# Kernel optimization log

Hardware: AMD Instinct MI355X
Metric: run time of the kernel (lower is better)

The kernel has to match this reference:

```python
import jax, jax.numpy as jnp
import numpy as np
from functools import partial

L, H, D, HD, V, S_MAX = 12, 12, 768, 64, 50257, 1024
EPS = 1e-5


def _layernorm(x, g, b):
    m = jnp.mean(x, axis=-1, keepdims=True)
    v = jnp.mean(jnp.square(x - m), axis=-1, keepdims=True)
    return (x - m) * jax.lax.rsqrt(v + EPS) * g + b


def setup_inputs() -> dict:
    key = jax.random.key(0)
    ks = jax.random.split(key, 8)
    s = 0.02
    return {
        "input_ids": jax.random.randint(ks[0], (2, 1024), 0, V),
        "wte": jax.random.normal(ks[1], (V, D), jnp.float32) * s,
        "wpe": jax.random.normal(ks[2], (S_MAX, D), jnp.float32) * s,
        "ln1_g": jnp.ones((L, D), jnp.float32),
        "ln1_b": jnp.zeros((L, D), jnp.float32),
        "Wqkv": jax.random.normal(ks[3], (L, D, 3 * D), jnp.float32) * s,
        "bqkv": jnp.zeros((L, 3 * D), jnp.float32),
        "Wo": jax.random.normal(ks[4], (L, D, D), jnp.float32) * s,
        "bo": jnp.zeros((L, D), jnp.float32),
        "ln2_g": jnp.ones((L, D), jnp.float32),
        "ln2_b": jnp.zeros((L, D), jnp.float32),
        "Wfc": jax.random.normal(ks[5], (L, D, 4 * D), jnp.float32) * s,
        "bfc": jnp.zeros((L, 4 * D), jnp.float32),
        "Wp": jax.random.normal(ks[6], (L, 4 * D, D), jnp.float32) * s,
        "bp": jnp.zeros((L, D), jnp.float32),
        "lnf_g": jnp.ones((D,), jnp.float32),
        "lnf_b": jnp.zeros((D,), jnp.float32),
    }


def reference(input_ids, wte, wpe, ln1_g, ln1_b, Wqkv, bqkv, Wo, bo,
              ln2_g, ln2_b, Wfc, bfc, Wp, bp, lnf_g, lnf_b):
    B, S = input_ids.shape
    x = wte[input_ids] + wpe[:S][None]  # [B,S,D] (embd dropout = identity in eval)
    causal = jnp.tril(jnp.ones((S, S), bool))  # [S,S]
    scale = 1.0 / jnp.sqrt(jnp.asarray(HD, x.dtype))

    def block(x, p):
        l1g, l1b, wqkv, bq, wo, bo_, l2g, l2b, wfc, bfc_, wp, bp_ = p
        h = _layernorm(x, l1g, l1b)
        qkv = h @ wqkv + bq  # [B,S,3D]
        q, k, v = jnp.split(qkv, 3, axis=-1)
        q = q.reshape(B, S, H, HD).transpose(0, 2, 1, 3)  # [B,H,S,HD]
        k = k.reshape(B, S, H, HD).transpose(0, 2, 1, 3)
        v = v.reshape(B, S, H, HD).transpose(0, 2, 1, 3)
        scores = jnp.einsum('bhqd,bhkd->bhqk', q, k) * scale  # [B,H,S,S]
        scores = jnp.where(causal, scores, -jnp.inf)
        attn = jax.nn.softmax(scores, axis=-1)  # attn dropout = identity in eval
        o = jnp.einsum('bhqk,bhkd->bhqd', attn, v)
        o = o.transpose(0, 2, 1, 3).reshape(B, S, D)
        x = x + (o @ wo + bo_)
        h2 = _layernorm(x, l2g, l2b)
        m = jax.nn.gelu(h2 @ wfc + bfc_, approximate=False)  # exact erf GELU
        x = x + (m @ wp + bp_)
        return x, None

    params = (ln1_g, ln1_b, Wqkv, bqkv, Wo, bo, ln2_g, ln2_b, Wfc, bfc, Wp, bp)
    x, _ = jax.lax.scan(block, x, params)
    x = _layernorm(x, lnf_g, lnf_b)
    logits = jnp.einsum('bsd,vd->bsv', x, wte)  # tied lm_head, no bias
    return logits
```

## Files before the change

### kernel.cpp

```cpp
#include <hip/hip_runtime.h>
#include <hip/hip_bf16.h>
#include <hip/hip_fp16.h>


typedef __attribute__((ext_vector_type(8))) short short8;
typedef __attribute__((ext_vector_type(4))) float f32x4;

#define S_LEN  1024
#define NTOK   2048
#define DMODEL 768
#define NHEAD  12
#define HEADD  64
#define NLAYER 12
#define VOCAB  50257
#define DQKV   2304
#define DFF    3072

__device__ __forceinline__ unsigned short f2bf(float f) {
  unsigned u = __float_as_uint(f);
  u += 0x7fffu + ((u >> 16) & 1u);
  return (unsigned short)(u >> 16);
}
__device__ __forceinline__ unsigned short f2h(float f) {
  __half h = __float2half(f);
  return *reinterpret_cast<unsigned short*>(&h);
}

__device__ __forceinline__ f32x4 mfma_bf16(short8 a, short8 b, f32x4 c) {
  asm("v_mfma_f32_16x16x32_bf16 %0, %1, %2, %0" : "+v"(c) : "v"(a), "v"(b));
  return c;
}
__device__ __forceinline__ f32x4 mfma_f16(short8 a, short8 b, f32x4 c) {
  asm("v_mfma_f32_16x16x32_f16 %0, %1, %2, %0" : "+v"(c) : "v"(a), "v"(b));
  return c;
}

__device__ __forceinline__ void gll16(const void* g, void* l) {
  __builtin_amdgcn_global_load_lds(
      (const __attribute__((address_space(1))) void*)g,
      (__attribute__((address_space(3))) void*)l, 16, 0, 0);
}

__global__ __launch_bounds__(256) void embed_kernel(
    const int* __restrict__ ids, const float* __restrict__ wte,
    const float* __restrict__ wpe, float* __restrict__ x) {
  int i = blockIdx.x * 256 + threadIdx.x;
  int n = i / DMODEL, d = i - n * DMODEL;
  int s = n & (S_LEN - 1);
  x[i] = wte[(long)ids[n] * DMODEL + d] + wpe[(long)s * DMODEL + d];
}

__global__ __launch_bounds__(256) void convert_kernel(
    const float* __restrict__ in, unsigned short* __restrict__ out, long n4) {
  long i = (long)blockIdx.x * 256 + threadIdx.x;
  if (i >= n4) return;
  float4 v = ((const float4*)in)[i];
  ushort4 r;
  r.x = f2bf(v.x); r.y = f2bf(v.y); r.z = f2bf(v.z); r.w = f2bf(v.w);
  ((ushort4*)out)[i] = r;
}

__global__ __launch_bounds__(256) void transpose_kernel(
    const float* __restrict__ in, unsigned short* __restrict__ out, int R, int C,
    long ldin, long ldout) {
  in  += (long)blockIdx.z * ldin;
  out += (long)blockIdx.z * ldout;
  __shared__ float tile[32][33];
  int tx = threadIdx.x & 31, ty = threadIdx.x >> 5;
  int c0 = blockIdx.x * 32, r0 = blockIdx.y * 32;
#pragma unroll
  for (int i = 0; i < 4; ++i) {
    int r = r0 + ty + i * 8;
    tile[ty + i * 8][tx] = in[(long)r * C + c0 + tx];
  }
  __syncthreads();
#pragma unroll
  for (int i = 0; i < 4; ++i) {
    int orow = c0 + ty + i * 8;
    out[(long)orow * R + r0 + tx] = f2bf(tile[tx][ty + i * 8]);
  }
}

__global__ __launch_bounds__(256) void ln_kernel(
    const float* __restrict__ x, const float* __restrict__ g,
    const float* __restrict__ b, unsigned short* __restrict__ out) {
  __shared__ float sb[4];
  int n = blockIdx.x, t = threadIdx.x;
  const float* xr = x + (long)n * DMODEL;
  float v0 = xr[t], v1 = xr[t + 256], v2 = xr[t + 512];
  float sum = v0 + v1 + v2;
#pragma unroll
  for (int o = 32; o; o >>= 1) sum += __shfl_xor(sum, o);
  if ((t & 63) == 0) sb[t >> 6] = sum;
  __syncthreads();
  sum = sb[0] + sb[1] + sb[2] + sb[3];
  float mean = sum * (1.f / 768.f);
  float d0 = v0 - mean, d1 = v1 - mean, d2 = v2 - mean;
  float vs = d0 * d0 + d1 * d1 + d2 * d2;
#pragma unroll
  for (int o = 32; o; o >>= 1) vs += __shfl_xor(vs, o);
  __syncthreads();
  if ((t & 63) == 0) sb[t >> 6] = vs;
  __syncthreads();
  vs = sb[0] + sb[1] + sb[2] + sb[3];
  float rs = rsqrtf(vs * (1.f / 768.f) + 1e-5f);
  out[(long)n * DMODEL + t]       = f2bf(d0 * rs * g[t] + b[t]);
  out[(long)n * DMODEL + t + 256] = f2bf(d1 * rs * g[t + 256] + b[t + 256]);
  out[(long)n * DMODEL + t + 512] = f2bf(d2 * rs * g[t + 512] + b[t + 512]);
}

__global__ __launch_bounds__(256) void attn_kernel(
    const unsigned short* __restrict__ qkv, unsigned short* __restrict__ o_out) {
  __shared__ __align__(16) unsigned short Ks[64 * 64];
  __shared__ __align__(16) unsigned short Vt[64 * 64];
  __shared__ __align__(16) unsigned short Ps[4][16 * 72];
  int t = threadIdx.x, w = t >> 6, l = t & 63;
  int qtile = blockIdx.x, bh = blockIdx.y;
  int b = bh / NHEAD, h = bh - b * NHEAD;
  long nb = (long)b * S_LEN;
  int g = l >> 4, lr = l & 15;

  int q0 = qtile * 64 + w * 16;
  const unsigned short* qrow = qkv + (nb + q0 + lr) * (long)DQKV + h * HEADD;
  short8 qf0 = *(const short8*)(qrow + g * 8);
  short8 qf1 = *(const short8*)(qrow + 32 + g * 8);

  f32x4 O[4];
  f32x4 zero = {0.f, 0.f, 0.f, 0.f};
#pragma unroll
  for (int jt = 0; jt < 4; ++jt) O[jt] = zero;
  float m[4] = {-INFINITY, -INFINITY, -INFINITY, -INFINITY};
  float ls[4] = {0.f, 0.f, 0.f, 0.f};

  int skey = t >> 2;
  int sd0 = (t & 3) * 16;
  int nt = qtile + 1;
  for (int c = 0; c < nt; ++c) {
    int k0 = c * 64;
    __syncthreads();
    {
      int c0 = t, row = c0 >> 3, j = c0 & 7;
      long goff = (nb + k0 + row) * (long)DQKV + DMODEL + h * HEADD + ((j ^ (row & 7)) * 8);
      gll16(qkv + goff, (char*)Ks + c0 * 16);
      int c1 = t + 256; row = c1 >> 3; j = c1 & 7;
      goff = (nb + k0 + row) * (long)DQKV + DMODEL + h * HEADD + ((j ^ (row & 7)) * 8);
      gll16(qkv + goff, (char*)Ks + c1 * 16);
    }
    {
      const unsigned short* vr =
          qkv + (nb + k0 + skey) * (long)DQKV + 2 * DMODEL + h * HEADD + sd0;
      short8 v0 = *(const short8*)vr;
      short8 v1 = *(const short8*)(vr + 8);
#pragma unroll
      for (int j = 0; j < 8; ++j) {
        int dv = sd0 + j;
        *(unsigned short*)((char*)Vt + dv * 128 + ((skey * 2) ^ ((dv & 7) << 4))) =
            (unsigned short)v0[j];
        dv = sd0 + 8 + j;
        *(unsigned short*)((char*)Vt + dv * 128 + ((skey * 2) ^ ((dv & 7) << 4))) =
            (unsigned short)v1[j];
      }
    }
    __syncthreads();

    f32x4 S[4];
#pragma unroll
    for (int kt = 0; kt < 4; ++kt) {
      int krow = kt * 16 + lr;
      int o0 = (g * 16) ^ ((krow & 7) << 4);
      int o1 = (64 + g * 16) ^ ((krow & 7) << 4);
      short8 kf0 = *(const short8*)((char*)Ks + krow * 128 + o0);
      short8 kf1 = *(const short8*)((char*)Ks + krow * 128 + o1);
      S[kt] = mfma_f16(qf0, kf0, zero);
      S[kt] = mfma_f16(qf1, kf1, S[kt]);
    }

    bool diag = (c == qtile);
    float sv[4][4];
#pragma unroll
    for (int kt = 0; kt < 4; ++kt)
#pragma unroll
      for (int r = 0; r < 4; ++r) {
        float xv = S[kt][r] * 0.125f;
        if (diag) {
          int key = kt * 16 + lr;
          int qq = w * 16 + g * 4 + r;
          if (key > qq) xv = -INFINITY;
        }
        sv[kt][r] = xv;
      }
    float nm[4], al[4];
#pragma unroll
    for (int r = 0; r < 4; ++r) {
      float mx = fmaxf(fmaxf(sv[0][r], sv[1][r]), fmaxf(sv[2][r], sv[3][r]));
#pragma unroll
      for (int o = 8; o; o >>= 1) mx = fmaxf(mx, __shfl_xor(mx, o));
      nm[r] = fmaxf(m[r], mx);
      al[r] = __expf(m[r] - nm[r]);
      m[r] = nm[r];
    }
    float rs[4] = {0.f, 0.f, 0.f, 0.f};
#pragma unroll
    for (int kt = 0; kt < 4; ++kt)
#pragma unroll
      for (int r = 0; r < 4; ++r) {
        float p = __expf(sv[kt][r] - nm[r]);
        rs[r] += p;
        Ps[w][(g * 4 + r) * 72 + kt * 16 + lr] = f2bf(p);
      }
#pragma unroll
    for (int r = 0; r < 4; ++r) {
#pragma unroll
      for (int o = 8; o; o >>= 1) rs[r] += __shfl_xor(rs[r], o);
      ls[r] = ls[r] * al[r] + rs[r];
    }
#pragma unroll
    for (int jt = 0; jt < 4; ++jt) {
      f32x4 ov = O[jt];
#pragma unroll
      for (int r = 0; r < 4; ++r) ov[r] *= al[r];
      O[jt] = ov;
    }
#pragma unroll
    for (int kk = 0; kk < 2; ++kk) {
      short8 pf = *(const short8*)(&Ps[w][lr * 72 + kk * 32 + g * 8]);
#pragma unroll
      for (int jt = 0; jt < 4; ++jt) {
        int dv = jt * 16 + lr;
        short8 vf = *(const short8*)((char*)Vt + dv * 128 +
                                     (((kk * 64 + g * 16)) ^ ((dv & 7) << 4)));
        O[jt] = mfma_bf16(pf, vf, O[jt]);
      }
    }
  }

  __syncthreads();
#pragma unroll
  for (int jt = 0; jt < 4; ++jt)
#pragma unroll
    for (int r = 0; r < 4; ++r) {
      int qq = w * 16 + g * 4 + r;
      int dv = jt * 16 + lr;
      *(unsigned short*)((char*)Ks + qq * 128 + ((dv * 2) ^ ((qq & 7) << 4))) =
          f2bf(O[jt][r] / ls[r]);
    }
  __syncthreads();
  {
    int qq = t >> 2, d0 = (t & 3) * 16;
    short8 o0 = *(const short8*)((char*)Ks + qq * 128 + ((d0 * 2) ^ ((qq & 7) << 4)));
    short8 o1 = *(const short8*)((char*)Ks + qq * 128 + (((d0 + 8) * 2) ^ ((qq & 7) << 4)));
    unsigned short* orow = o_out + (nb + qtile * 64 + qq) * (long)DMODEL + h * HEADD + d0;
    *(short8*)orow = o0;
    *(short8*)(orow + 8) = o1;
  }
}

template <int TM, int TN, int HAS_BIAS, int ACT_GELU, int RESID, int OUT_BF16,
          int OUT_QKV, int COLG, int GRIDSWAP, int XCDSWZ>
__global__ __launch_bounds__(TM == 128 ? 256 : 128) void gemm_bt_kernel(
    const short* __restrict__ A, const short* __restrict__ Bt,
    const float* __restrict__ bias, float* __restrict__ Cf,
    unsigned short* __restrict__ Cb, int K, int Nv) {
  __shared__ __align__(16) short As[TM * 32];
  __shared__ __align__(16) short Bs[TN * 32];
  constexpr int NJ = (TN == 64) ? 2 : 4;
  constexpr int WN = (TN == 64) ? 32 : 64;
  int t = threadIdx.x;
  int lane = t & 63, wave = t >> 6;
  int wm = (TM == 128) ? (wave >> 1) : 0;
  int wn = (TM == 128) ? (wave & 1) : wave;

  int bx = blockIdx.x, by = blockIdx.y;
  if (XCDSWZ) {
    int gx = gridDim.x;
    int nwg = gx * gridDim.y;
    int wg = by * gx + bx;
    int q8 = nwg >> 3, r8 = nwg & 7;
    int xcd = wg & 7, idx = wg >> 3;
    int nid = (xcd < r8 ? xcd * (q8 + 1) : r8 * (q8 + 1) + (xcd - r8) * q8) + idx;
    bx = nid % gx;
    by = nid / gx;
  }
  int row0 = (GRIDSWAP ? bx : by) * TM;
  int col0 = (GRIDSWAP ? by : bx) * TN;
  int lr = lane & 15, lk = (lane >> 4) * 8;

  f32x4 acc[4][NJ];
  f32x4 zero = {0.f, 0.f, 0.f, 0.f};
#pragma unroll
  for (int i = 0; i < 4; ++i)
#pragma unroll
    for (int j = 0; j < NJ; ++j) acc[i][j] = zero;

  int rr = t >> 2, k8 = (t & 3) * 8;

  if (TM == 128) {
    int ar0 = row0 + rr, ar1 = ar0 + 64;
    int br0 = col0 + rr, br1 = br0 + 64;
    if (COLG) { br0 = min(br0, Nv - 1); br1 = min(br1, Nv - 1); }
    const short* Ap0 = A + (long)ar0 * K + k8;
    const short* Ap1 = A + (long)ar1 * K + k8;
    const short* Bp0 = Bt + (long)br0 * K + k8;
    const short* Bp1 = Bt + (long)br1 * K + k8;
    for (int kt = 0; kt < K; kt += 32) {
      __syncthreads();
      gll16(Ap0 + kt, (char*)As + t * 16);
      gll16(Ap1 + kt, (char*)As + 4096 + t * 16);
      gll16(Bp0 + kt, (char*)Bs + t * 16);
      gll16(Bp1 + kt, (char*)Bs + 4096 + t * 16);
      __syncthreads();
      short8 af[4], bfr[4];
#pragma unroll
      for (int i = 0; i < 4; ++i) {
        af[i]  = *(const short8*)(As + (wm * 64 + i * 16 + lr) * 32 + lk);
        bfr[i] = *(const short8*)(Bs + (wn * 64 + i * 16 + lr) * 32 + lk);
      }
#pragma unroll
      for (int i = 0; i < 4; ++i)
#pragma unroll
        for (int j = 0; j < 4; ++j)
          acc[i][j] = mfma_bf16(af[i], bfr[j], acc[i][j]);
    }
  } else if (TN == 128) {
    const short* Ap = A + (long)(row0 + rr) * K + k8;
    const short* Bp = Bt + (long)(col0 + rr) * K + k8;
    for (int kt = 0; kt < K; kt += 32) {
      __syncthreads();
      gll16(Ap + kt, (char*)As + t * 16);
      gll16(Ap + (long)32 * K + kt, (char*)As + 2048 + t * 16);
      gll16(Bp + kt, (char*)Bs + t * 16);
      gll16(Bp + (long)32 * K + kt, (char*)Bs + 2048 + t * 16);
      gll16(Bp + (long)64 * K + kt, (char*)Bs + 4096 + t * 16);
      gll16(Bp + (long)96 * K + kt, (char*)Bs + 6144 + t * 16);
      __syncthreads();
      short8 af[4], bfr[4];
#pragma unroll
      for (int i = 0; i < 4; ++i) {
        af[i]  = *(const short8*)(As + (i * 16 + lr) * 32 + lk);
        bfr[i] = *(const short8*)(Bs + (wn * 64 + i * 16 + lr) * 32 + lk);
      }
#pragma unroll
      for (int i = 0; i < 4; ++i)
#pragma unroll
        for (int j = 0; j < 4; ++j)
          acc[i][j] = mfma_bf16(af[i], bfr[j], acc[i][j]);
    }
  } else {
    const short* Ap = A + (long)(row0 + rr) * K + k8;
    const short* Bp = Bt + (long)(col0 + rr) * K + k8;
    for (int kt = 0; kt < K; kt += 32) {
      __syncthreads();
      gll16(Ap + kt, (char*)As + t * 16);
      gll16(Ap + (long)32 * K + kt, (char*)As + 2048 + t * 16);
      gll16(Bp + kt, (char*)Bs + t * 16);
      gll16(Bp + (long)32 * K + kt, (char*)Bs + 2048 + t * 16);
      __syncthreads();
      short8 af[4], bfr[2];
#pragma unroll
      for (int i = 0; i < 4; ++i)
        af[i] = *(const short8*)(As + (i * 16 + lr) * 32 + lk);
#pragma unroll
      for (int j = 0; j < 2; ++j)
        bfr[j] = *(const short8*)(Bs + (wn * 32 + j * 16 + lr) * 32 + lk);
#pragma unroll
      for (int i = 0; i < 4; ++i)
#pragma unroll
        for (int j = 0; j < 2; ++j)
          acc[i][j] = mfma_bf16(af[i], bfr[j], acc[i][j]);
    }
  }

  int orow = row0 + wm * 64 + (lane >> 4) * 4;
  int ocol = col0 + wn * WN + lr;
#pragma unroll
  for (int i = 0; i < 4; ++i) {
#pragma unroll
    for (int j = 0; j < NJ; ++j) {
      int col = ocol + j * 16;
      if (COLG && col >= Nv) continue;
      float bv = 0.f;
      if (HAS_BIAS) bv = bias[col];
#pragma unroll
      for (int r = 0; r < 4; ++r) {
        float xv = acc[i][j][r] + bv;
        if (ACT_GELU) xv = 0.5f * xv * (1.f + erff(xv * 0.70710678118654752f));
        long idx = (long)(orow + i * 16 + r) * Nv + col;
        if (RESID) {
          Cf[idx] += xv;
        } else if (OUT_QKV) {
          Cb[idx] = (col < 2 * DMODEL) ? f2h(xv) : f2bf(xv);
        } else if (OUT_BF16) {
          Cb[idx] = f2bf(xv);
        } else {
          Cf[idx] = xv;
        }
      }
    }
  }
}

extern "C" void kernel_launch(void* const* d_in, const int* in_sizes, int n_in,
                              void* d_out, int out_size, void* d_ws, size_t ws_size,
                              hipStream_t stream) {
  const int*   ids  = (const int*)d_in[0];
  const float* wte  = (const float*)d_in[1];
  const float* wpe  = (const float*)d_in[2];
  const float* ln1g = (const float*)d_in[3];
  const float* ln1b = (const float*)d_in[4];
  const float* Wqkv = (const float*)d_in[5];
  const float* bqkv = (const float*)d_in[6];
  const float* Wo   = (const float*)d_in[7];
  const float* bo   = (const float*)d_in[8];
  const float* ln2g = (const float*)d_in[9];
  const float* ln2b = (const float*)d_in[10];
  const float* Wfc  = (const float*)d_in[11];
  const float* bfc  = (const float*)d_in[12];
  const float* Wp   = (const float*)d_in[13];
  const float* bp   = (const float*)d_in[14];
  const float* lnfg = (const float*)d_in[15];
  const float* lnfb = (const float*)d_in[16];
  float* out = (float*)d_out;

  size_t off = 0;
  auto carve = [&](size_t bytes) {
    void* p = (char*)d_ws + off;
    off += (bytes + 255) & ~(size_t)255;
    return p;
  };
  float* x = (float*)carve((size_t)NTOK * DMODEL * 4);
  unsigned short* qkvb = (unsigned short*)carve((size_t)NTOK * DQKV * 2);
  unsigned short* h    = (unsigned short*)carve((size_t)NTOK * DMODEL * 2);
  unsigned short* ob   = (unsigned short*)carve((size_t)NTOK * DMODEL * 2);
  unsigned short* mb   = (unsigned short*)carve((size_t)NTOK * DFF * 2);
  unsigned short* wteb = (unsigned short*)carve((size_t)VOCAB * DMODEL * 2);

  const size_t szQ = (size_t)DMODEL * DQKV * 2, szO = (size_t)DMODEL * DMODEL * 2;
  const size_t szF = (size_t)DMODEL * DFF * 2,  szP = (size_t)DFF * DMODEL * 2;
  size_t fixed_end = off;
  size_t full_need = fixed_end + NLAYER * (szQ + szO + szF + szP) + 4 * 256;
  bool full = ws_size >= full_need;

  unsigned short *tQ, *tO, *tF, *tP;
  if (full) {
    tQ = (unsigned short*)carve(NLAYER * szQ);
    tO = (unsigned short*)carve(NLAYER * szO);
    tF = (unsigned short*)carve(NLAYER * szF);
    tP = (unsigned short*)carve(NLAYER * szP);
  } else {
    tQ = (unsigned short*)carve(szQ);
    tO = (unsigned short*)carve(szO);
    tF = (unsigned short*)carve(szF);
    tP = (unsigned short*)carve(szP);
  }
  if (off > ws_size) return;

  dim3 blk(256), blk128(128);
  long n4 = (long)VOCAB * DMODEL / 4;
  convert_kernel<<<dim3((unsigned)((n4 + 255) / 256)), blk, 0, stream>>>(wte, wteb, n4);
  embed_kernel<<<dim3(NTOK * DMODEL / 256), blk, 0, stream>>>(ids, wte, wpe, x);

  if (full) {
    transpose_kernel<<<dim3(DQKV / 32, DMODEL / 32, NLAYER), blk, 0, stream>>>(
        Wqkv, tQ, DMODEL, DQKV, (long)DMODEL * DQKV, (long)DMODEL * DQKV);
    transpose_kernel<<<dim3(DMODEL / 32, DMODEL / 32, NLAYER), blk, 0, stream>>>(
        Wo, tO, DMODEL, DMODEL, (long)DMODEL * DMODEL, (long)DMODEL * DMODEL);
    transpose_kernel<<<dim3(DFF / 32, DMODEL / 32, NLAYER), blk, 0, stream>>>(
        Wfc, tF, DMODEL, DFF, (long)DMODEL * DFF, (long)DMODEL * DFF);
    transpose_kernel<<<dim3(DMODEL / 32, DFF / 32, NLAYER), blk, 0, stream>>>(
        Wp, tP, DFF, DMODEL, (long)DFF * DMODEL, (long)DFF * DMODEL);
  }

  for (int l = 0; l < NLAYER; ++l) {
    const unsigned short* tQl = tQ + (full ? (size_t)l * DMODEL * DQKV : 0);
    const unsigned short* tOl = tO + (full ? (size_t)l * DMODEL * DMODEL : 0);
    const unsigned short* tFl = tF + (full ? (size_t)l * DMODEL * DFF : 0);
    const unsigned short* tPl = tP + (full ? (size_t)l * DFF * DMODEL : 0);
    if (!full) {
      transpose_kernel<<<dim3(DQKV / 32, DMODEL / 32), blk, 0, stream>>>(
          Wqkv + (long)l * DMODEL * DQKV, tQ, DMODEL, DQKV, 0, 0);
      transpose_kernel<<<dim3(DMODEL / 32, DMODEL / 32), blk, 0, stream>>>(
          Wo + (long)l * DMODEL * DMODEL, tO, DMODEL, DMODEL, 0, 0);
      transpose_kernel<<<dim3(DFF / 32, DMODEL / 32), blk, 0, stream>>>(
          Wfc + (long)l * DMODEL * DFF, tF, DMODEL, DFF, 0, 0);
      transpose_kernel<<<dim3(DMODEL / 32, DFF / 32), blk, 0, stream>>>(
          Wp + (long)l * DFF * DMODEL, tP, DFF, DMODEL, 0, 0);
    }

    ln_kernel<<<dim3(NTOK), blk, 0, stream>>>(x, ln1g + l * DMODEL, ln1b + l * DMODEL, h);
    gemm_bt_kernel<64, 128, 1, 0, 0, 0, 1, 0, 0, 0>
        <<<dim3(DQKV / 128, NTOK / 64), blk128, 0, stream>>>(
        (const short*)h, (const short*)tQl, bqkv + (long)l * DQKV,
        nullptr, qkvb, DMODEL, DQKV);

    attn_kernel<<<dim3(S_LEN / 64, 2 * NHEAD), blk, 0, stream>>>(qkvb, ob);

    gemm_bt_kernel<64, 64, 1, 0, 1, 0, 0, 0, 0, 0>
        <<<dim3(DMODEL / 64, NTOK / 64), blk128, 0, stream>>>(
        (const short*)ob, (const short*)tOl, bo + (long)l * DMODEL,
        x, nullptr, DMODEL, DMODEL);

    ln_kernel<<<dim3(NTOK), blk, 0, stream>>>(x, ln2g + l * DMODEL, ln2b + l * DMODEL, h);
    gemm_bt_kernel<64, 128, 1, 1, 0, 1, 0, 0, 0, 0>
        <<<dim3(DFF / 128, NTOK / 64), blk128, 0, stream>>>(
        (const short*)h, (const short*)tFl, bfc + (long)l * DFF,
        nullptr, mb, DMODEL, DFF);

    gemm_bt_kernel<64, 64, 1, 0, 1, 0, 0, 0, 0, 0>
        <<<dim3(DMODEL / 64, NTOK / 64), blk128, 0, stream>>>(
        (const short*)mb, (const short*)tPl, bp + (long)l * DMODEL,
        x, nullptr, DFF, DMODEL);
  }

  ln_kernel<<<dim3(NTOK), blk, 0, stream>>>(x, lnfg, lnfb, h);
  gemm_bt_kernel<128, 128, 0, 0, 0, 0, 0, 1, 1, 1>
      <<<dim3(NTOK / 128, (VOCAB + 127) / 128), blk, 0, stream>>>(
      (const short*)h, (const short*)wteb, nullptr, out, nullptr, DMODEL, VOCAB);
}
```

Baseline: 2.560 ms.

## Use fp16 for attention PV and load two K-slices per GEMM barrier

```diff
diff --git a/kernel.cpp b/kernel.cpp
--- a/kernel.cpp
+++ b/kernel.cpp
@@ -206,7 +206,7 @@
       for (int r = 0; r < 4; ++r) {
         float p = __expf(sv[kt][r] - nm[r]);
         rs[r] += p;
-        Ps[w][(g * 4 + r) * 72 + kt * 16 + lr] = f2bf(p);
+        Ps[w][(g * 4 + r) * 72 + kt * 16 + lr] = f2h(p);
       }
 #pragma unroll
     for (int r = 0; r < 4; ++r) {
@@ -229,7 +229,7 @@
         int dv = jt * 16 + lr;
         short8 vf = *(const short8*)((char*)Vt + dv * 128 +
                                      (((kk * 64 + g * 16)) ^ ((dv & 7) << 4)));
-        O[jt] = mfma_bf16(pf, vf, O[jt]);
+        O[jt] = mfma_f16(pf, vf, O[jt]);
       }
     }
   }
@@ -256,13 +256,13 @@
 }
 
 template <int TM, int TN, int HAS_BIAS, int ACT_GELU, int RESID, int OUT_BF16,
-          int OUT_QKV, int COLG, int GRIDSWAP, int XCDSWZ>
+          int OUT_F16, int COLG, int GRIDSWAP, int XCDSWZ>
 __global__ __launch_bounds__(TM == 128 ? 256 : 128) void gemm_bt_kernel(
     const short* __restrict__ A, const short* __restrict__ Bt,
     const float* __restrict__ bias, float* __restrict__ Cf,
     unsigned short* __restrict__ Cb, int K, int Nv) {
-  __shared__ __align__(16) short As[TM * 32];
-  __shared__ __align__(16) short Bs[TN * 32];
+  __shared__ __align__(16) short As[2][TM * 32];
+  __shared__ __align__(16) short Bs[2][TN * 32];
   constexpr int NJ = (TN == 64) ? 2 : 4;
   constexpr int WN = (TN == 64) ? 32 : 64;
   int t = threadIdx.x;
@@ -302,71 +302,92 @@
     const short* Ap1 = A + (long)ar1 * K + k8;
     const short* Bp0 = Bt + (long)br0 * K + k8;
     const short* Bp1 = Bt + (long)br1 * K + k8;
-    for (int kt = 0; kt < K; kt += 32) {
+    for (int kt = 0; kt < K; kt += 64) {
       __syncthreads();
-      gll16(Ap0 + kt, (char*)As + t * 16);
-      gll16(Ap1 + kt, (char*)As + 4096 + t * 16);
-      gll16(Bp0 + kt, (char*)Bs + t * 16);
-      gll16(Bp1 + kt, (char*)Bs + 4096 + t * 16);
+      gll16(Ap0 + kt, (char*)As[0] + t * 16);
+      gll16(Ap1 + kt, (char*)As[0] + 4096 + t * 16);
+      gll16(Bp0 + kt, (char*)Bs[0] + t * 16);
+      gll16(Bp1 + kt, (char*)Bs[0] + 4096 + t * 16);
+      gll16(Ap0 + kt + 32, (char*)As[1] + t * 16);
+      gll16(Ap1 + kt + 32, (char*)As[1] + 4096 + t * 16);
+      gll16(Bp0 + kt + 32, (char*)Bs[1] + t * 16);
+      gll16(Bp1 + kt + 32, (char*)Bs[1] + 4096 + t * 16);
       __syncthreads();
-      short8 af[4], bfr[4];
-#pragma unroll
-      for (int i = 0; i < 4; ++i) {
-        af[i]  = *(const short8*)(As + (wm * 64 + i * 16 + lr) * 32 + lk);
-        bfr[i] = *(const short8*)(Bs + (wn * 64 + i * 16 + lr) * 32 + lk);
-      }
-#pragma unroll
-      for (int i = 0; i < 4; ++i)
-#pragma unroll
-        for (int j = 0; j < 4; ++j)
-          acc[i][j] = mfma_bf16(af[i], bfr[j], acc[i][j]);
+#pragma unroll
+      for (int s = 0; s < 2; ++s) {
+        short8 af[4], bfr[4];
+#pragma unroll
+        for (int i = 0; i < 4; ++i) {
+          af[i]  = *(const short8*)(As[s] + (wm * 64 + i * 16 + lr) * 32 + lk);
+          bfr[i] = *(const short8*)(Bs[s] + (wn * 64 + i * 16 + lr) * 32 + lk);
+        }
+#pragma unroll
+        for (int i = 0; i < 4; ++i)
+#pragma unroll
+          for (int j = 0; j < 4; ++j)
+            acc[i][j] = mfma_bf16(af[i], bfr[j], acc[i][j]);
+      }
     }
   } else if (TN == 128) {
     const short* Ap = A + (long)(row0 + rr) * K + k8;
     const short* Bp = Bt + (long)(col0 + rr) * K + k8;
-    for (int kt = 0; kt < K; kt += 32) {
+    for (int kt = 0; kt < K; kt += 64) {
       __syncthreads();
-      gll16(Ap + kt, (char*)As + t * 16);
-      gll16(Ap + (long)32 * K + kt, (char*)As + 2048 + t * 16);
-      gll16(Bp + kt, (char*)Bs + t * 16);
-      gll16(Bp + (long)32 * K + kt, (char*)Bs + 2048 + t * 16);
-      gll16(Bp + (long)64 * K + kt, (char*)Bs + 4096 + t * 16);
-      gll16(Bp + (long)96 * K + kt, (char*)Bs + 6144 + t * 16);
+#pragma unroll
+      for (int s = 0; s < 2; ++s) {
+        int ko = kt + s * 32;
+        gll16(Ap + ko, (char*)As[s] + t * 16);
+        gll16(Ap + (long)32 * K + ko, (char*)As[s] + 2048 + t * 16);
+        gll16(Bp + ko, (char*)Bs[s] + t * 16);
+        gll16(Bp + (long)32 * K + ko, (char*)Bs[s] + 2048 + t * 16);
+        gll16(Bp + (long)64 * K + ko, (char*)Bs[s] + 4096 + t * 16);
+        gll16(Bp + (long)96 * K + ko, (char*)Bs[s] + 6144 + t * 16);
+      }
       __syncthreads();
-      short8 af[4], bfr[4];
-#pragma unroll
-      for (int i = 0; i < 4; ++i) {
-        af[i]  = *(const short8*)(As + (i * 16 + lr) * 32 + lk);
-        bfr[i] = *(const short8*)(Bs + (wn * 64 + i * 16 + lr) * 32 + lk);
-      }
-#pragma unroll
-      for (int i = 0; i < 4; ++i)
-#pragma unroll
-        for (int j = 0; j < 4; ++j)
-          acc[i][j] = mfma_bf16(af[i], bfr[j], acc[i][j]);
+#pragma unroll
+      for (int s = 0; s < 2; ++s) {
+        short8 af[4], bfr[4];
+#pragma unroll
+        for (int i = 0; i < 4; ++i) {
+          af[i]  = *(const short8*)(As[s] + (i * 16 + lr) * 32 + lk);
+          bfr[i] = *(const short8*)(Bs[s] + (wn * 64 + i * 16 + lr) * 32 + lk);
+        }
+#pragma unroll
+        for (int i = 0; i < 4; ++i)
+#pragma unroll
+          for (int j = 0; j < 4; ++j)
+            acc[i][j] = mfma_bf16(af[i], bfr[j], acc[i][j]);
+      }
     }
   } else {
     const short* Ap = A + (long)(row0 + rr) * K + k8;
     const short* Bp = Bt + (long)(col0 + rr) * K + k8;
-    for (int kt = 0; kt < K; kt += 32) {
+    for (int kt = 0; kt < K; kt += 64) {
       __syncthreads();
-      gll16(Ap + kt, (char*)As + t * 16);
-      gll16(Ap + (long)32 * K + kt, (char*)As + 2048 + t * 16);
-      gll16(Bp + kt, (char*)Bs + t * 16);
-      gll16(Bp + (long)32 * K + kt, (char*)Bs + 2048 + t * 16);
+#pragma unroll
+      for (int s = 0; s < 2; ++s) {
+        int ko = kt + s * 32;
+        gll16(Ap + ko, (char*)As[s] + t * 16);
+        gll16(Ap + (long)32 * K + ko, (char*)As[s] + 2048 + t * 16);
+        gll16(Bp + ko, (char*)Bs[s] + t * 16);
+        gll16(Bp + (long)32 * K + ko, (char*)Bs[s] + 2048 + t * 16);
+      }
       __syncthreads();
-      short8 af[4], bfr[2];
-#pragma unroll
-      for (int i = 0; i < 4; ++i)
-        af[i] = *(const short8*)(As + (i * 16 + lr) * 32 + lk);
-#pragma unroll
-      for (int j = 0; j < 2; ++j)
-        bfr[j] = *(const short8*)(Bs + (wn * 32 + j * 16 + lr) * 32 + lk);
-#pragma unroll
-      for (int i = 0; i < 4; ++i)
+#pragma unroll
+      for (int s = 0; s < 2; ++s) {
+        short8 af[4], bfr[2];
+#pragma unroll
+        for (int i = 0; i < 4; ++i)
+          af[i] = *(const short8*)(As[s] + (i * 16 + lr) * 32 + lk);
 #pragma unroll
         for (int j = 0; j < 2; ++j)
-          acc[i][j] = mfma_bf16(af[i], bfr[j], acc[i][j]);
+          bfr[j] = *(const short8*)(Bs[s] + (wn * 32 + j * 16 + lr) * 32 + lk);
+#pragma unroll
+        for (int i = 0; i < 4; ++i)
+#pragma unroll
+          for (int j = 0; j < 2; ++j)
+            acc[i][j] = mfma_bf16(af[i], bfr[j], acc[i][j]);
+      }
     }
   }
 
@@ -387,8 +408,8 @@
         long idx = (long)(orow + i * 16 + r) * Nv + col;
         if (RESID) {
           Cf[idx] += xv;
-        } else if (OUT_QKV) {
-          Cb[idx] = (col < 2 * DMODEL) ? f2h(xv) : f2bf(xv);
+        } else if (OUT_F16) {
+          Cb[idx] = f2h(xv);
         } else if (OUT_BF16) {
           Cb[idx] = f2bf(xv);
         } else {
```

Measured after the change: 2.279 ms. -11.0%, faster.
